# Optimization experiments

Hardware: AMD Instinct MI355X
Metric: run time of the kernel (lower is better)

The kernel has to match this reference:

```python
import jax, jax.numpy as jnp
import numpy as np

TOP_K = 2
NUM_EXPERTS = 64


def setup_inputs() -> dict:
    key = jax.random.key(0)
    k1, k2, k3 = jax.random.split(key, 3)
    T, D, E = 16384, 2048, NUM_EXPERTS
    x = jax.random.normal(k1, (T, D), dtype=jnp.float32)
    # gate projection weight (the _forward of the concrete router)
    w_gate = jax.random.normal(k2, (D, E), dtype=jnp.float32) * (1.0 / np.sqrt(D))
    # gate.perturbation(scores.shape, NORMAL): additive Gaussian noise, materialized for determinism
    noise = jax.random.normal(k3, (T, E), dtype=jnp.float32)
    return {"x": x, "w_gate": w_gate, "noise": noise}


def reference(x, w_gate, noise):
    T, E = x.shape[0], w_gate.shape[1]
    # _forward: expert scores [T, E]
    scores = x @ w_gate
    # gate.compute on perturbed scores: softmax -> top-k -> renormalized gates
    probs = jax.nn.softmax(scores + noise, axis=-1)
    topk_vals, topk_idx = jax.lax.top_k(probs, TOP_K)          # [T, k]
    gates = topk_vals / jnp.sum(topk_vals, axis=-1, keepdims=True)
    # combine tensor [T, E]: gate weight scattered to the chosen experts
    rows = jnp.arange(T)[:, None]                               # [T, 1]
    combine = jnp.zeros((T, E), dtype=gates.dtype).at[rows, topk_idx].add(gates)
    # _track_expert_activations: scatter_add of ones per selected expert column
    expert_activation = jnp.zeros((E,), dtype=jnp.float32).at[topk_idx.ravel()].add(1.0)
    return combine, topk_idx, gates, expert_activation
```

## Files before the change

### kernel.cpp

```cpp
#include <hip/hip_runtime.h>
#include <math.h>

#define T_TOKENS 16384
#define DIM      2048
#define NEXP     64
#define TOPK     2

#define NKC   4
#define NEG   4
#define EPG   (NEXP / NEG)
#define KC    (DIM / NKC)
#define PSTR  68

#define OFF_COMBINE 0
#define OFF_IDX     (T_TOKENS * NEXP)
#define OFF_GATES   (OFF_IDX + T_TOKENS * TOPK)
#define OFF_ACT     (OFF_GATES + T_TOKENS * TOPK)

__global__ void zero_act_kernel(float* __restrict__ out) {
    int i = threadIdx.x;
    if (i < NEXP) out[OFF_ACT + i] = 0.0f;
}

struct Acc { float4 a0, a1, a2, a3; };

__device__ __forceinline__ void fma16(Acc& A, float xs, const float* __restrict__ wr) {
    const float4 w0 = *reinterpret_cast<const float4*>(wr + 0);
    const float4 w1 = *reinterpret_cast<const float4*>(wr + 4);
    const float4 w2 = *reinterpret_cast<const float4*>(wr + 8);
    const float4 w3 = *reinterpret_cast<const float4*>(wr + 12);
    A.a0.x = fmaf(xs, w0.x, A.a0.x); A.a0.y = fmaf(xs, w0.y, A.a0.y);
    A.a0.z = fmaf(xs, w0.z, A.a0.z); A.a0.w = fmaf(xs, w0.w, A.a0.w);
    A.a1.x = fmaf(xs, w1.x, A.a1.x); A.a1.y = fmaf(xs, w1.y, A.a1.y);
    A.a1.z = fmaf(xs, w1.z, A.a1.z); A.a1.w = fmaf(xs, w1.w, A.a1.w);
    A.a2.x = fmaf(xs, w2.x, A.a2.x); A.a2.y = fmaf(xs, w2.y, A.a2.y);
    A.a2.z = fmaf(xs, w2.z, A.a2.z); A.a2.w = fmaf(xs, w2.w, A.a2.w);
    A.a3.x = fmaf(xs, w3.x, A.a3.x); A.a3.y = fmaf(xs, w3.y, A.a3.y);
    A.a3.z = fmaf(xs, w3.z, A.a3.z); A.a3.w = fmaf(xs, w3.w, A.a3.w);
}

__device__ __forceinline__ void fma16x4(Acc& A, float4 xv, const float* __restrict__ wr) {
    fma16(A, xv.x, wr);
    fma16(A, xv.y, wr + NEXP);
    fma16(A, xv.z, wr + 2 * NEXP);
    fma16(A, xv.w, wr + 3 * NEXP);
}

__global__ __launch_bounds__(1024, 4)
void router_kernel(const float* __restrict__ x,
                   const float* __restrict__ w,
                   const float* __restrict__ noise,
                   float* __restrict__ out) {
    __shared__ float part[NKC][64][PSTR];
    __shared__ float nsh[64][PSTR];
    __shared__ float g1s[64], g2s[64];
    __shared__ int   i1s[64], i2s[64];
    __shared__ float bins[NEXP];

    const int tid  = threadIdx.x;
    const int lane = tid & 63;
    const int wv   = __builtin_amdgcn_readfirstlane(tid >> 6);
    const int eg   = wv & (NEG - 1);
    const int kc   = wv >> 2;
    const int row  = blockIdx.x * 64 + lane;
    const int k0   = kc * KC;

    if (tid < NEXP) bins[tid] = 0.0f;

    {
        const int r = tid >> 4, c = (tid & 15) * 4;
        const float4 nv = *reinterpret_cast<const float4*>(
            noise + (size_t)(blockIdx.x * 64 + r) * NEXP + c);
        *reinterpret_cast<float4*>(&nsh[r][c]) = nv;
    }

    Acc A;
    A.a0 = make_float4(0.f, 0.f, 0.f, 0.f);
    A.a1 = A.a0; A.a2 = A.a0; A.a3 = A.a0;

    const float* __restrict__ xp = x + (size_t)row * DIM + k0;
    const float* __restrict__ wp = w + (size_t)k0 * NEXP + eg * EPG;

    float4 X0 = *reinterpret_cast<const float4*>(xp + 0);
    float4 X1 = *reinterpret_cast<const float4*>(xp + 4);
    float4 X2 = *reinterpret_cast<const float4*>(xp + 8);
    float4 X3 = *reinterpret_cast<const float4*>(xp + 12);
    float4 Y0 = *reinterpret_cast<const float4*>(xp + 16);
    float4 Y1 = *reinterpret_cast<const float4*>(xp + 20);
    float4 Y2 = *reinterpret_cast<const float4*>(xp + 24);
    float4 Y3 = *reinterpret_cast<const float4*>(xp + 28);

    #pragma unroll 1
    for (int kk = 0; kk < KC; kk += 16) {
        const int kpre = (kk + 32 < KC) ? (kk + 32) : 0;
        const float4 Z0 = *reinterpret_cast<const float4*>(xp + kpre + 0);
        const float4 Z1 = *reinterpret_cast<const float4*>(xp + kpre + 4);
        const float4 Z2 = *reinterpret_cast<const float4*>(xp + kpre + 8);
        const float4 Z3 = *reinterpret_cast<const float4*>(xp + kpre + 12);

        const float* __restrict__ wr = wp + (size_t)kk * NEXP;
        fma16x4(A, X0, wr);
        fma16x4(A, X1, wr + 4 * NEXP);
        fma16x4(A, X2, wr + 8 * NEXP);
        fma16x4(A, X3, wr + 12 * NEXP);

        X0 = Y0; X1 = Y1; X2 = Y2; X3 = Y3;
        Y0 = Z0; Y1 = Z1; Y2 = Z2; Y3 = Z3;
    }

    {
        float* pr = &part[kc][lane][eg * EPG];
        *reinterpret_cast<float4*>(pr + 0)  = A.a0;
        *reinterpret_cast<float4*>(pr + 4)  = A.a1;
        *reinterpret_cast<float4*>(pr + 8)  = A.a2;
        *reinterpret_cast<float4*>(pr + 12) = A.a3;
    }
    __syncthreads();

    if (wv == 0) {
        const int r = lane;
        float m1 = -1e30f, m2 = -1e30f;
        int i1 = 0, i2 = 0;
        #pragma unroll
        for (int j = 0; j < NEXP; j += 4) {
            float4 s        = *reinterpret_cast<const float4*>(&part[0][r][j]);
            const float4 p1 = *reinterpret_cast<const float4*>(&part[1][r][j]);
            const float4 p2 = *reinterpret_cast<const float4*>(&part[2][r][j]);
            const float4 p3 = *reinterpret_cast<const float4*>(&part[3][r][j]);
            const float4 nv = *reinterpret_cast<const float4*>(&nsh[r][j]);
            s.x += p1.x + p2.x + p3.x + nv.x;
            s.y += p1.y + p2.y + p3.y + nv.y;
            s.z += p1.z + p2.z + p3.z + nv.z;
            s.w += p1.w + p2.w + p3.w + nv.w;
            if (s.x > m1) { m2 = m1; i2 = i1; m1 = s.x; i1 = j + 0; } else if (s.x > m2) { m2 = s.x; i2 = j + 0; }
            if (s.y > m1) { m2 = m1; i2 = i1; m1 = s.y; i1 = j + 1; } else if (s.y > m2) { m2 = s.y; i2 = j + 1; }
            if (s.z > m1) { m2 = m1; i2 = i1; m1 = s.z; i1 = j + 2; } else if (s.z > m2) { m2 = s.z; i2 = j + 2; }
            if (s.w > m1) { m2 = m1; i2 = i1; m1 = s.w; i1 = j + 3; } else if (s.w > m2) { m2 = s.w; i2 = j + 3; }
        }

        const float t  = expf(m2 - m1);
        const float g1 = 1.0f / (1.0f + t);
        const float g2 = 1.0f - g1;

        out[OFF_IDX + row * 2 + 0]   = (float)i1;
        out[OFF_IDX + row * 2 + 1]   = (float)i2;
        out[OFF_GATES + row * 2 + 0] = g1;
        out[OFF_GATES + row * 2 + 1] = g2;

        g1s[r] = g1; g2s[r] = g2; i1s[r] = i1; i2s[r] = i2;
        atomicAdd(&bins[i1], 1.0f);
        atomicAdd(&bins[i2], 1.0f);
    }
    __syncthreads();

    {
        const int r = tid >> 4, c = (tid & 15) * 4;
        const int   a  = i1s[r], b = i2s[r];
        const float ga = g1s[r], gb = g2s[r];
        float4 v;
        v.x = (c + 0 == a) ? ga : (c + 0 == b) ? gb : 0.0f;
        v.y = (c + 1 == a) ? ga : (c + 1 == b) ? gb : 0.0f;
        v.z = (c + 2 == a) ? ga : (c + 2 == b) ? gb : 0.0f;
        v.w = (c + 3 == a) ? ga : (c + 3 == b) ? gb : 0.0f;
        *reinterpret_cast<float4*>(
            out + OFF_COMBINE + (size_t)(blockIdx.x * 64 + r) * NEXP + c) = v;
    }

    if (tid < NEXP) {
        const float v = bins[tid];
        if (v != 0.0f) atomicAdd(out + OFF_ACT + tid, v);
    }
}

extern "C" void kernel_launch(void* const* d_in, const int* in_sizes, int n_in,
                              void* d_out, int out_size, void* d_ws, size_t ws_size,
                              hipStream_t stream) {
    const float* x     = (const float*)d_in[0];
    const float* wg    = (const float*)d_in[1];
    const float* noise = (const float*)d_in[2];
    float* out = (float*)d_out;

    zero_act_kernel<<<1, 64, 0, stream>>>(out);
    router_kernel<<<T_TOKENS / 64, 1024, 0, stream>>>(x, wg, noise, out);
}
```

Measured before the change: 245.1 us.

## Compute gate projection with split-bf16 MFMA emulating fp32 precision

Replaces the scalar fp32 FMA GEMV with bf16 MFMA 16x16x32 instructions, splitting each fp32 operand into three bf16 terms and accumulating six cross products to approximate fp32 accuracy. A preprocessing kernel splits and transposes the weight matrix into three bf16 planes in a device global buffer, and also zeroes the activation counts. The main kernel drops to 256 threads per block with no k-split partial reduction. This moves the compute onto matrix cores at the cost of six MFMAs per tile and on-the-fly conversion of x, and the dropped low-order cross terms can change top-k ties.

```diff
diff --git a/kernel.cpp b/kernel.cpp
--- a/kernel.cpp
+++ b/kernel.cpp
@@ -1,4 +1,5 @@
 #include <hip/hip_runtime.h>
+#include <hip/hip_bf16.h>
 #include <math.h>
 
 #define T_TOKENS 16384
@@ -6,136 +7,171 @@
 #define NEXP     64
 #define TOPK     2
 
-#define NKC   4
-#define NEG   4
-#define EPG   (NEXP / NEG)
-#define KC    (DIM / NKC)
-#define PSTR  68
-
 #define OFF_COMBINE 0
 #define OFF_IDX     (T_TOKENS * NEXP)
 #define OFF_GATES   (OFF_IDX + T_TOKENS * TOPK)
 #define OFF_ACT     (OFF_GATES + T_TOKENS * TOPK)
 
-__global__ void zero_act_kernel(float* __restrict__ out) {
-    int i = threadIdx.x;
-    if (i < NEXP) out[OFF_ACT + i] = 0.0f;
-}
-
-struct Acc { float4 a0, a1, a2, a3; };
-
-__device__ __forceinline__ void fma16(Acc& A, float xs, const float* __restrict__ wr) {
-    const float4 w0 = *reinterpret_cast<const float4*>(wr + 0);
-    const float4 w1 = *reinterpret_cast<const float4*>(wr + 4);
-    const float4 w2 = *reinterpret_cast<const float4*>(wr + 8);
-    const float4 w3 = *reinterpret_cast<const float4*>(wr + 12);
-    A.a0.x = fmaf(xs, w0.x, A.a0.x); A.a0.y = fmaf(xs, w0.y, A.a0.y);
-    A.a0.z = fmaf(xs, w0.z, A.a0.z); A.a0.w = fmaf(xs, w0.w, A.a0.w);
-    A.a1.x = fmaf(xs, w1.x, A.a1.x); A.a1.y = fmaf(xs, w1.y, A.a1.y);
-    A.a1.z = fmaf(xs, w1.z, A.a1.z); A.a1.w = fmaf(xs, w1.w, A.a1.w);
-    A.a2.x = fmaf(xs, w2.x, A.a2.x); A.a2.y = fmaf(xs, w2.y, A.a2.y);
-    A.a2.z = fmaf(xs, w2.z, A.a2.z); A.a2.w = fmaf(xs, w2.w, A.a2.w);
-    A.a3.x = fmaf(xs, w3.x, A.a3.x); A.a3.y = fmaf(xs, w3.y, A.a3.y);
-    A.a3.z = fmaf(xs, w3.z, A.a3.z); A.a3.w = fmaf(xs, w3.w, A.a3.w);
-}
-
-__device__ __forceinline__ void fma16x4(Acc& A, float4 xv, const float* __restrict__ wr) {
-    fma16(A, xv.x, wr);
-    fma16(A, xv.y, wr + NEXP);
-    fma16(A, xv.z, wr + 2 * NEXP);
-    fma16(A, xv.w, wr + 3 * NEXP);
-}
-
-__global__ __launch_bounds__(1024, 4)
+#define PSTR 68
+#define WT_PLANE (NEXP * DIM)
+
+typedef __attribute__((ext_vector_type(8))) short  short8;
+typedef __attribute__((ext_vector_type(4))) float  f32x4;
+
+#define MFMA16(a, b, c) __builtin_amdgcn_mfma_f32_16x16x32_bf16((a), (b), (c), 0, 0, 0)
+
+__device__ __align__(16) unsigned short g_wt[3 * WT_PLANE];
+
+__device__ __forceinline__ unsigned short bf16_bits(__hip_bfloat16 h) {
+    return __builtin_bit_cast(unsigned short, h);
+}
+
+__global__ void wsplit_kernel(const float* __restrict__ w,
+                              float* __restrict__ out) {
+    const int tid = threadIdx.x;
+    if (blockIdx.x == 0 && tid < NEXP) out[OFF_ACT + tid] = 0.0f;
+
+    const int krow = blockIdx.x * 16 + (tid >> 4);
+    const int e0   = (tid & 15) * 4;
+    const float4 v = *reinterpret_cast<const float4*>(w + (size_t)krow * NEXP + e0);
+    const float f[4] = {v.x, v.y, v.z, v.w};
+    #pragma unroll
+    for (int m = 0; m < 4; ++m) {
+        const int e  = e0 + m;
+        const float val = f[m];
+        const __hip_bfloat16 h  = __float2bfloat16(val);
+        const float r1          = val - __bfloat162float(h);
+        const __hip_bfloat16 mm = __float2bfloat16(r1);
+        const float r2          = r1 - __bfloat162float(mm);
+        const __hip_bfloat16 lo = __float2bfloat16(r2);
+        g_wt[(size_t)e * DIM + krow]                = bf16_bits(h);
+        g_wt[(size_t)e * DIM + krow + WT_PLANE]     = bf16_bits(mm);
+        g_wt[(size_t)e * DIM + krow + 2 * WT_PLANE] = bf16_bits(lo);
+    }
+}
+
+__global__ __launch_bounds__(256, 1)
 void router_kernel(const float* __restrict__ x,
-                   const float* __restrict__ w,
                    const float* __restrict__ noise,
                    float* __restrict__ out) {
-    __shared__ float part[NKC][64][PSTR];
+    __shared__ float part[64][PSTR];
     __shared__ float nsh[64][PSTR];
     __shared__ float g1s[64], g2s[64];
     __shared__ int   i1s[64], i2s[64];
     __shared__ float bins[NEXP];
 
     const int tid  = threadIdx.x;
-    const int lane = tid & 63;
-    const int wv   = __builtin_amdgcn_readfirstlane(tid >> 6);
-    const int eg   = wv & (NEG - 1);
-    const int kc   = wv >> 2;
-    const int row  = blockIdx.x * 64 + lane;
-    const int k0   = kc * KC;
+    const int l    = tid & 63;
+    const int wv   = tid >> 6;
+    const int lrow = l & 15;
+    const int lk   = l >> 4;
+    const int brow = blockIdx.x * 64;
 
     if (tid < NEXP) bins[tid] = 0.0f;
 
-    {
-        const int r = tid >> 4, c = (tid & 15) * 4;
-        const float4 nv = *reinterpret_cast<const float4*>(
-            noise + (size_t)(blockIdx.x * 64 + r) * NEXP + c);
-        *reinterpret_cast<float4*>(&nsh[r][c]) = nv;
-    }
-
-    Acc A;
-    A.a0 = make_float4(0.f, 0.f, 0.f, 0.f);
-    A.a1 = A.a0; A.a2 = A.a0; A.a3 = A.a0;
-
-    const float* __restrict__ xp = x + (size_t)row * DIM + k0;
-    const float* __restrict__ wp = w + (size_t)k0 * NEXP + eg * EPG;
-
-    float4 X0 = *reinterpret_cast<const float4*>(xp + 0);
-    float4 X1 = *reinterpret_cast<const float4*>(xp + 4);
-    float4 X2 = *reinterpret_cast<const float4*>(xp + 8);
-    float4 X3 = *reinterpret_cast<const float4*>(xp + 12);
-    float4 Y0 = *reinterpret_cast<const float4*>(xp + 16);
-    float4 Y1 = *reinterpret_cast<const float4*>(xp + 20);
-    float4 Y2 = *reinterpret_cast<const float4*>(xp + 24);
-    float4 Y3 = *reinterpret_cast<const float4*>(xp + 28);
-
-    #pragma unroll 1
-    for (int kk = 0; kk < KC; kk += 16) {
-        const int kpre = (kk + 32 < KC) ? (kk + 32) : 0;
-        const float4 Z0 = *reinterpret_cast<const float4*>(xp + kpre + 0);
-        const float4 Z1 = *reinterpret_cast<const float4*>(xp + kpre + 4);
-        const float4 Z2 = *reinterpret_cast<const float4*>(xp + kpre + 8);
-        const float4 Z3 = *reinterpret_cast<const float4*>(xp + kpre + 12);
-
-        const float* __restrict__ wr = wp + (size_t)kk * NEXP;
-        fma16x4(A, X0, wr);
-        fma16x4(A, X1, wr + 4 * NEXP);
-        fma16x4(A, X2, wr + 8 * NEXP);
-        fma16x4(A, X3, wr + 12 * NEXP);
-
-        X0 = Y0; X1 = Y1; X2 = Y2; X3 = Y3;
-        Y0 = Z0; Y1 = Z1; Y2 = Z2; Y3 = Z3;
-    }
-
-    {
-        float* pr = &part[kc][lane][eg * EPG];
-        *reinterpret_cast<float4*>(pr + 0)  = A.a0;
-        *reinterpret_cast<float4*>(pr + 4)  = A.a1;
-        *reinterpret_cast<float4*>(pr + 8)  = A.a2;
-        *reinterpret_cast<float4*>(pr + 12) = A.a3;
+    #pragma unroll
+    for (int i = 0; i < 4; ++i) {
+        const int idx = tid + i * 256;
+        const int r = idx >> 4, c = (idx & 15) * 4;
+        *reinterpret_cast<float4*>(&nsh[r][c]) =
+            *reinterpret_cast<const float4*>(noise + (size_t)(brow + r) * NEXP + c);
+    }
+
+    const float* xa = x + (size_t)(brow + wv * 16 + lrow) * DIM + lk * 8;
+    const unsigned short* wb[4];
+    #pragma unroll
+    for (int n = 0; n < 4; ++n)
+        wb[n] = g_wt + (size_t)(n * 16 + lrow) * DIM + lk * 8;
+
+    f32x4 acc[4];
+    #pragma unroll
+    for (int n = 0; n < 4; ++n) acc[n] = (f32x4){0.0f, 0.0f, 0.0f, 0.0f};
+
+    float4 XA[4][2];
+    short8 WH[2][4], WM[2][4], WL[2][4];
+
+    #pragma unroll
+    for (int s = 0; s < 4; ++s) {
+        XA[s][0] = *reinterpret_cast<const float4*>(xa + s * 32);
+        XA[s][1] = *reinterpret_cast<const float4*>(xa + s * 32 + 4);
+    }
+    #pragma unroll
+    for (int s = 0; s < 2; ++s) {
+        #pragma unroll
+        for (int n = 0; n < 4; ++n) {
+            WH[s][n] = *reinterpret_cast<const short8*>(wb[n] + s * 32);
+            WM[s][n] = *reinterpret_cast<const short8*>(wb[n] + s * 32 + WT_PLANE);
+            WL[s][n] = *reinterpret_cast<const short8*>(wb[n] + s * 32 + 2 * WT_PLANE);
+        }
+    }
+
+    #pragma unroll 4
+    for (int s = 0; s < 64; ++s) {
+        const int sa = s & 3;
+        const int su = s & 1;
+
+        float xr[8];
+        xr[0] = XA[sa][0].x; xr[1] = XA[sa][0].y; xr[2] = XA[sa][0].z; xr[3] = XA[sa][0].w;
+        xr[4] = XA[sa][1].x; xr[5] = XA[sa][1].y; xr[6] = XA[sa][1].z; xr[7] = XA[sa][1].w;
+        short8 ah, am, al;
+        #pragma unroll
+        for (int i = 0; i < 8; ++i) {
+            const float f0 = xr[i];
+            const __hip_bfloat16 h  = __float2bfloat16(f0);
+            const float r1          = f0 - __bfloat162float(h);
+            const __hip_bfloat16 m  = __float2bfloat16(r1);
+            const float r2          = r1 - __bfloat162float(m);
+            const __hip_bfloat16 lo = __float2bfloat16(r2);
+            ah[i] = (short)bf16_bits(h);
+            am[i] = (short)bf16_bits(m);
+            al[i] = (short)bf16_bits(lo);
+        }
+
+        const int sA = (s + 4 < 64) ? (s + 4) : 63;
+        XA[sa][0] = *reinterpret_cast<const float4*>(xa + sA * 32);
+        XA[sa][1] = *reinterpret_cast<const float4*>(xa + sA * 32 + 4);
+
+        #pragma unroll
+        for (int n = 0; n < 4; ++n) {
+            acc[n] = MFMA16(ah, WH[su][n], acc[n]);
+            acc[n] = MFMA16(ah, WM[su][n], acc[n]);
+            acc[n] = MFMA16(am, WH[su][n], acc[n]);
+            acc[n] = MFMA16(ah, WL[su][n], acc[n]);
+            acc[n] = MFMA16(am, WM[su][n], acc[n]);
+            acc[n] = MFMA16(al, WH[su][n], acc[n]);
+        }
+
+        const int sW = (s + 2 < 64) ? (s + 2) : s;
+        #pragma unroll
+        for (int n = 0; n < 4; ++n) {
+            WH[su][n] = *reinterpret_cast<const short8*>(wb[n] + sW * 32);
+            WM[su][n] = *reinterpret_cast<const short8*>(wb[n] + sW * 32 + WT_PLANE);
+            WL[su][n] = *reinterpret_cast<const short8*>(wb[n] + sW * 32 + 2 * WT_PLANE);
+        }
+    }
+
+    #pragma unroll
+    for (int n = 0; n < 4; ++n) {
+        #pragma unroll
+        for (int j = 0; j < 4; ++j)
+            part[wv * 16 + lk * 4 + j][n * 16 + lrow] = acc[n][j];
     }
     __syncthreads();
 
     if (wv == 0) {
-        const int r = lane;
+        const int r   = l;
+        const int row = brow + r;
         float m1 = -1e30f, m2 = -1e30f;
         int i1 = 0, i2 = 0;
         #pragma unroll
         for (int j = 0; j < NEXP; j += 4) {
-            float4 s        = *reinterpret_cast<const float4*>(&part[0][r][j]);
-            const float4 p1 = *reinterpret_cast<const float4*>(&part[1][r][j]);
-            const float4 p2 = *reinterpret_cast<const float4*>(&part[2][r][j]);
-            const float4 p3 = *reinterpret_cast<const float4*>(&part[3][r][j]);
+            float4 s4       = *reinterpret_cast<const float4*>(&part[r][j]);
             const float4 nv = *reinterpret_cast<const float4*>(&nsh[r][j]);
-            s.x += p1.x + p2.x + p3.x + nv.x;
-            s.y += p1.y + p2.y + p3.y + nv.y;
-            s.z += p1.z + p2.z + p3.z + nv.z;
-            s.w += p1.w + p2.w + p3.w + nv.w;
-            if (s.x > m1) { m2 = m1; i2 = i1; m1 = s.x; i1 = j + 0; } else if (s.x > m2) { m2 = s.x; i2 = j + 0; }
-            if (s.y > m1) { m2 = m1; i2 = i1; m1 = s.y; i1 = j + 1; } else if (s.y > m2) { m2 = s.y; i2 = j + 1; }
-            if (s.z > m1) { m2 = m1; i2 = i1; m1 = s.z; i1 = j + 2; } else if (s.z > m2) { m2 = s.z; i2 = j + 2; }
-            if (s.w > m1) { m2 = m1; i2 = i1; m1 = s.w; i1 = j + 3; } else if (s.w > m2) { m2 = s.w; i2 = j + 3; }
+            s4.x += nv.x; s4.y += nv.y; s4.z += nv.z; s4.w += nv.w;
+            if (s4.x > m1) { m2 = m1; i2 = i1; m1 = s4.x; i1 = j + 0; } else if (s4.x > m2) { m2 = s4.x; i2 = j + 0; }
+            if (s4.y > m1) { m2 = m1; i2 = i1; m1 = s4.y; i1 = j + 1; } else if (s4.y > m2) { m2 = s4.y; i2 = j + 1; }
+            if (s4.z > m1) { m2 = m1; i2 = i1; m1 = s4.z; i1 = j + 2; } else if (s4.z > m2) { m2 = s4.z; i2 = j + 2; }
+            if (s4.w > m1) { m2 = m1; i2 = i1; m1 = s4.w; i1 = j + 3; } else if (s4.w > m2) { m2 = s4.w; i2 = j + 3; }
         }
 
         const float t  = expf(m2 - m1);
@@ -153,8 +189,10 @@
     }
     __syncthreads();
 
-    {
-        const int r = tid >> 4, c = (tid & 15) * 4;
+    #pragma unroll
+    for (int i = 0; i < 4; ++i) {
+        const int idx = tid + i * 256;
+        const int r = idx >> 4, c = (idx & 15) * 4;
         const int   a  = i1s[r], b = i2s[r];
         const float ga = g1s[r], gb = g2s[r];
         float4 v;
@@ -163,7 +201,7 @@
         v.z = (c + 2 == a) ? ga : (c + 2 == b) ? gb : 0.0f;
         v.w = (c + 3 == a) ? ga : (c + 3 == b) ? gb : 0.0f;
         *reinterpret_cast<float4*>(
-            out + OFF_COMBINE + (size_t)(blockIdx.x * 64 + r) * NEXP + c) = v;
+            out + OFF_COMBINE + (size_t)(brow + r) * NEXP + c) = v;
     }
 
     if (tid < NEXP) {
@@ -180,6 +218,6 @@
     const float* noise = (const float*)d_in[2];
     float* out = (float*)d_out;
 
-    zero_act_kernel<<<1, 64, 0, stream>>>(out);
-    router_kernel<<<T_TOKENS / 64, 1024, 0, stream>>>(x, wg, noise, out);
-}
+    wsplit_kernel<<<DIM / 16, 256, 0, stream>>>(wg, out);
+    router_kernel<<<T_TOKENS / 64, 256, 0, stream>>>(x, noise, out);
+}
```

Measured after the change: 308.5 us. +25.9%, slower.
